# Kernel tuning notes

Measured on AMD Instinct MI355X. Metric: run time of the kernel, lower is better.

## Reference

```python
import jax, jax.numpy as jnp
import numpy as np

M = 2_097_152
C = 32
R = 256

# Same plane_axes buffer as the torch module (3 permutation matrices).
PLANE_AXES = jnp.array(
    [[[0, 1, 0], [1, 0, 0], [0, 0, 1]],
     [[0, 0, 1], [1, 0, 0], [0, 1, 0]],
     [[0, 1, 0], [0, 0, 1], [1, 0, 0]]], dtype=jnp.float32)


def setup_inputs() -> dict:
    key = jax.random.key(0)
    k1, k2 = jax.random.split(key)
    xyz = jax.random.uniform(k1, (M, 3), dtype=jnp.float32, minval=-1.0, maxval=1.0)
    # rand_init: triplane = randn * 0.001
    triplane = jax.random.normal(k2, (3, C, R, R), dtype=jnp.float32) * 0.001
    return {"xyz": xyz, "triplane": triplane}


def _grid_sample_bilinear(plane, coords):
    """plane: (C,H,W); coords: (M,2) normalized (x,y) in [-1,1].
    Matches torch F.grid_sample(mode='bilinear', padding_mode='zeros',
    align_corners=True). Returns (M,C)."""
    Cc, H, W = plane.shape
    ix = (coords[:, 0] + 1.0) * 0.5 * (W - 1)  # x indexes width
    iy = (coords[:, 1] + 1.0) * 0.5 * (H - 1)  # y indexes height
    x0 = jnp.floor(ix)
    y0 = jnp.floor(iy)
    x1 = x0 + 1.0
    y1 = y0 + 1.0
    wx1 = ix - x0
    wx0 = 1.0 - wx1
    wy1 = iy - y0
    wy0 = 1.0 - wy1

    def tap(xf, yf, w):
        valid = (xf >= 0) & (xf <= W - 1) & (yf >= 0) & (yf <= H - 1)
        xi = jnp.clip(xf, 0, W - 1).astype(jnp.int32)
        yi = jnp.clip(yf, 0, H - 1).astype(jnp.int32)
        v = plane[:, yi, xi]  # (C, M) gather
        return v * (w * valid.astype(w.dtype))[None, :]

    out = (tap(x0, y0, wx0 * wy0) + tap(x1, y0, wx1 * wy0)
           + tap(x0, y1, wx0 * wy1) + tap(x1, y1, wx1 * wy1))  # (C, M)
    return out.T  # (M, C)


def reference(xyz, triplane):
    # project_onto_planes: xyz @ inv(plane_axes), keep first two coords
    inv_planes = jnp.linalg.inv(PLANE_AXES)             # (3,3,3)
    proj = jnp.einsum('md,pdk->pmk', xyz, inv_planes)[..., :2]  # (3,M,2)
    feats = jax.vmap(_grid_sample_bilinear)(triplane, proj)      # (3,M,C)
    return feats.sum(axis=0)  # (M,C)
```

## Files before the change

### kernel.cpp

```cpp
#include <hip/hip_runtime.h>

#define R 256
#define C 32
#define NBIN 512
#define CAPB 6144
#define PPB 1024
#define CNTP 16
#define SUBC 64

typedef float f32x4 __attribute__((ext_vector_type(4)));

__device__ __forceinline__ void bin_key_of(float px, float py, float pz,
                                           int& bin, int& key) {
    int gx = min(max((int)((px + 1.0f) * 16.0f), 0), 31);
    int gy = min(max((int)((py + 1.0f) * 16.0f), 0), 31);
    int gz = min(max((int)((pz + 1.0f) * 16.0f), 0), 31);
    int bx = gx >> 2, by = gy >> 2, bz = gz >> 2;
    int oct = ((bz >> 2) << 2) | ((by >> 2) << 1) | (bx >> 2);
    int sub = ((bz & 3) << 4) | ((by & 3) << 2) | (bx & 3);
    bin = (sub << 3) | oct;
    key = ((gz & 3) << 4) | ((gy & 3) << 2) | (gx & 3);
}

__device__ __forceinline__ void convert_body(const float* __restrict__ tri,
                                             ushort* __restrict__ tw, int bid) {
    int p = bid >> 8;
    int y = bid & (R - 1);
    int x = threadIdx.x;

    unsigned packed[C / 2];
#pragma unroll
    for (int i = 0; i < C / 2; ++i) {
        unsigned w = 0;
#pragma unroll
        for (int h = 0; h < 2; ++h) {
            float f = tri[(((p * C + (2 * i + h)) * R) + y) * R + x];
            unsigned u = __float_as_uint(f);
            unsigned r = (u + 0x7fffu + ((u >> 16) & 1u)) >> 16;
            w |= (r & 0xffffu) << (16 * h);
        }
        packed[i] = w;
    }
    uint4* dst = (uint4*)(tw + ((size_t)(p * R + y) * R + x) * C);
#pragma unroll
    for (int i = 0; i < 4; ++i) {
        dst[i] = make_uint4(packed[4 * i], packed[4 * i + 1],
                            packed[4 * i + 2], packed[4 * i + 3]);
    }
}

__global__ __launch_bounds__(256) void convert_scatter_kernel(
        const float* __restrict__ tri, ushort* __restrict__ tw,
        const float* __restrict__ xyz, unsigned* __restrict__ acnt,
        unsigned* __restrict__ ovcnt, f32x4* __restrict__ arena,
        f32x4* __restrict__ ov, int M) {
    int bid = blockIdx.x;
    if (bid < 3 * R) {
        convert_body(tri, tw, bid);
        return;
    }

    __shared__ unsigned lcnt[NBIN], lbase[NBIN], gbase[NBIN], lofs[NBIN];
    __shared__ f32x4 stag[PPB];
    __shared__ ushort sbin[PPB];

    int t = threadIdx.x;
    for (int c = t; c < NBIN; c += 256) { lcnt[c] = 0u; lofs[c] = 0u; }
    __syncthreads();

    int base = (bid - 3 * R) * PPB;
    float pxl[4], pyl[4], pzl[4];
    int   bl[4], kl[4];
#pragma unroll
    for (int k = 0; k < 4; ++k) {
        int m = base + k * 256 + t;
        bl[k] = -1;
        if (m < M) {
            pxl[k] = xyz[3 * m + 0];
            pyl[k] = xyz[3 * m + 1];
            pzl[k] = xyz[3 * m + 2];
            bin_key_of(pxl[k], pyl[k], pzl[k], bl[k], kl[k]);
            atomicAdd(&lcnt[bl[k]], 1u);
        }
    }
    __syncthreads();

    if (t < 64) {
        unsigned run = 0;
        for (int c = 0; c < NBIN; c += 64) {
            unsigned x   = lcnt[c + t];
            unsigned inc = x;
#pragma unroll
            for (int d = 1; d < 64; d <<= 1) {
                unsigned v = __shfl_up(inc, d);
                if (t >= d) inc += v;
            }
            lbase[c + t] = run + inc - x;
            run += __shfl(inc, 63);
        }
    }
    __syncthreads();

    for (int c = t; c < NBIN; c += 256) {
        unsigned x = lcnt[c];
        if (x) gbase[c] = atomicAdd(&acnt[c * CNTP], x);
    }
    __syncthreads();

#pragma unroll
    for (int k = 0; k < 4; ++k) {
        if (bl[k] >= 0) {
            unsigned j = lbase[bl[k]] + atomicAdd(&lofs[bl[k]], 1u);
            int m = base + k * 256 + t;
            f32x4 rec = {pxl[k], pyl[k], pzl[k],
                         __int_as_float((kl[k] << 21) | m)};
            stag[j] = rec;
            sbin[j] = (ushort)bl[k];
        }
    }
    __syncthreads();

    int tot = (int)(lbase[NBIN - 1] + lcnt[NBIN - 1]);
    for (int j = t; j < tot; j += 256) {
        int b = sbin[j];
        unsigned pos = gbase[b] + ((unsigned)j - lbase[b]);
        f32x4 rec = stag[j];
        if (pos < CAPB) arena[(size_t)b * CAPB + pos] = rec;
        else            ov[atomicAdd(ovcnt, 1u)] = rec;
    }
}

__global__ __launch_bounds__(256) void convert_kernel(const float* __restrict__ tri,
                                                      ushort* __restrict__ tw) {
    convert_body(tri, tw, blockIdx.x);
}

__device__ __forceinline__ void tap_fma(uint4 v, float w, float* acc) {
    unsigned d[4] = {v.x, v.y, v.z, v.w};
#pragma unroll
    for (int k = 0; k < 4; ++k) {
        acc[2 * k]     = fmaf(w, __uint_as_float(d[k] << 16),          acc[2 * k]);
        acc[2 * k + 1] = fmaf(w, __uint_as_float(d[k] & 0xffff0000u), acc[2 * k + 1]);
    }
}

__device__ __forceinline__ void sample_point(float px, float py, float pz, int mo,
                                             const ushort* __restrict__ twc,
                                             float* __restrict__ out, int cq) {
    float uu[3] = {py, pz, py};
    float vv[3] = {px, px, pz};

    uint4 v[12];
    float wt[12];
#pragma unroll
    for (int p = 0; p < 3; ++p) {
        float ix = (uu[p] + 1.0f) * 0.5f * 255.0f;
        float iy = (vv[p] + 1.0f) * 0.5f * 255.0f;
        int   x0 = (int)ix;
        int   y0 = (int)iy;
        float wx1 = ix - (float)x0;
        float wy1 = iy - (float)y0;
        float wx0 = 1.0f - wx1;
        float wy0 = 1.0f - wy1;
        int x1 = min(x0 + 1, R - 1);
        int y1 = min(y0 + 1, R - 1);

        const ushort* pl = twc + (size_t)p * R * R * C;
        v[4 * p + 0] = *(const uint4*)(pl + (y0 * R + x0) * C);
        v[4 * p + 1] = *(const uint4*)(pl + (y0 * R + x1) * C);
        v[4 * p + 2] = *(const uint4*)(pl + (y1 * R + x0) * C);
        v[4 * p + 3] = *(const uint4*)(pl + (y1 * R + x1) * C);
        wt[4 * p + 0] = wx0 * wy0;
        wt[4 * p + 1] = wx1 * wy0;
        wt[4 * p + 2] = wx0 * wy1;
        wt[4 * p + 3] = wx1 * wy1;
    }

    float acc[8];
#pragma unroll
    for (int j = 0; j < 8; ++j) acc[j] = 0.0f;
#pragma unroll
    for (int s = 0; s < 12; ++s) tap_fma(v[s], wt[s], acc);

    f32x4* o = (f32x4*)(out + (size_t)mo * C + 8 * cq);
    f32x4 o0 = {acc[0], acc[1], acc[2], acc[3]};
    f32x4 o1 = {acc[4], acc[5], acc[6], acc[7]};
    __builtin_nontemporal_store(o0, o);
    __builtin_nontemporal_store(o1, o + 1);
}

__global__ __launch_bounds__(512, 4) void sample_bins(
        const f32x4* __restrict__ arena, const unsigned* __restrict__ acnt,
        const unsigned* __restrict__ ovcnt, const f32x4* __restrict__ ov,
        const ushort* __restrict__ tw, float* __restrict__ out) {
    __shared__ unsigned char skey[CAPB];
    __shared__ ushort        sidx[CAPB];
    __shared__ unsigned      scnt[SUBC], sbase[SUBC], sofs[SUBC];

    int bin = blockIdx.x;
    int t   = threadIdx.x;

    if (t < SUBC) { scnt[t] = 0u; sofs[t] = 0u; }
    __syncthreads();

    int n = min((int)acnt[bin * CNTP], CAPB);
    const f32x4* bk = arena + (size_t)bin * CAPB;

    for (int i = t; i < n; i += 512) {
        int bits = __float_as_int(bk[i].w);
        int k    = (bits >> 21) & 63;
        skey[i]  = (unsigned char)k;
        atomicAdd(&scnt[k], 1u);
    }
    __syncthreads();

    if (t < 64) {
        unsigned x   = scnt[t];
        unsigned inc = x;
#pragma unroll
        for (int d = 1; d < 64; d <<= 1) {
            unsigned v = __shfl_up(inc, d);
            if (t >= d) inc += v;
        }
        sbase[t] = inc - x;
    }
    __syncthreads();

    for (int i = t; i < n; i += 512) {
        int k = skey[i];
        unsigned pos = sbase[k] + atomicAdd(&sofs[k], 1u);
        sidx[pos] = (ushort)i;
    }
    __syncthreads();

    int quad = t >> 2;
    int cq   = t & 3;
    const ushort* twc = tw + 8 * cq;

    for (int j0 = 0; j0 < n; j0 += 128) {
        int j = j0 + quad;
        if (j < n) {
            f32x4 r = bk[sidx[j]];
            int mo = __float_as_int(r.w) & 0x1FFFFF;
            sample_point(r.x, r.y, r.z, mo, twc, out, cq);
        }
    }

    int nov = (int)*ovcnt;
    if (nov > 0) {
        int gq = (bin * 512 + t) >> 2;
        for (int j = gq; j < nov; j += 512 * 128) {
            f32x4 r = ov[j];
            int mo = __float_as_int(r.w) & 0x1FFFFF;
            sample_point(r.x, r.y, r.z, mo, twc, out, cq);
        }
    }
}

__global__ __launch_bounds__(256) void sample_kernel(const float* __restrict__ xyz,
                                                     const ushort* __restrict__ tw,
                                                     float* __restrict__ out, int M) {
    int tid = blockIdx.x * 256 + threadIdx.x;
    int q   = tid >> 2;
    int cq  = tid & 3;
    int nq  = (gridDim.x * 256) >> 2;
    const ushort* twc = tw + 8 * cq;
    for (int m = q; m < M; m += nq) {
        float px = xyz[3 * m + 0], py = xyz[3 * m + 1], pz = xyz[3 * m + 2];
        sample_point(px, py, pz, m, twc, out, cq);
    }
}

extern "C" void kernel_launch(void* const* d_in, const int* in_sizes, int n_in,
                              void* d_out, int out_size, void* d_ws, size_t ws_size,
                              hipStream_t stream) {
    const float* xyz = (const float*)d_in[0];
    const float* tri = (const float*)d_in[1];
    float* out = (float*)d_out;

    int M = in_sizes[0] / 3;

    size_t tw_bytes  = (size_t)3 * R * R * C * sizeof(ushort);
    size_t cnt_off   = tw_bytes;
    size_t cnt_bytes = (size_t)NBIN * CNTP * sizeof(unsigned) + 128;
    size_t arena_off = cnt_off + ((cnt_bytes + 255) & ~(size_t)255);
    size_t ov_off    = arena_off + (size_t)NBIN * CAPB * sizeof(f32x4);
    size_t need      = ov_off + (size_t)M * sizeof(f32x4);

    ushort*   tw    = (ushort*)d_ws;
    unsigned* acnt  = (unsigned*)((char*)d_ws + cnt_off);
    unsigned* ovcnt = acnt + NBIN * CNTP;
    f32x4*    arena = (f32x4*)((char*)d_ws + arena_off);
    f32x4*    ov    = (f32x4*)((char*)d_ws + ov_off);

    if (ws_size >= need) {
        hipMemsetAsync(acnt, 0, cnt_bytes, stream);
        int sb = (M + PPB - 1) / PPB;
        convert_scatter_kernel<<<3 * R + sb, 256, 0, stream>>>(
            tri, tw, xyz, acnt, ovcnt, arena, ov, M);
        sample_bins<<<NBIN, 512, 0, stream>>>(arena, acnt, ovcnt, ov, tw, out);
    } else {
        convert_kernel<<<3 * R, 256, 0, stream>>>(tri, tw);
        sample_kernel<<<4096, 256, 0, stream>>>(xyz, tw, out, M);
    }
}
```

Measured before the change: 437.1 us.

## Stage sorted bin records in LDS and enlarge scatter blocks to 1024 threads

The binning pass now uses 1024-thread blocks that each handle 4096 points, and triplane conversion covers four rows per block. This cuts the number of global bin-counter atomics and produces longer contiguous runs when writing to the arena. The sampling kernel now copies full records into shared memory in sub-key order, rather than keeping an index array and re-reading the arena from global memory at random. In exchange, both kernels use much more LDS (about 74 KB for the sampler's record buffer), which can lower occupancy. Bins larger than the shared capacity fall back to unsorted processing, and the fast path now also requires M to be a multiple of 4096.

```diff
diff --git a/kernel.cpp b/kernel.cpp
--- a/kernel.cpp
+++ b/kernel.cpp
@@ -4,9 +4,10 @@
 #define C 32
 #define NBIN 512
 #define CAPB 6144
-#define PPB 1024
+#define PPB 4096
 #define CNTP 16
 #define SUBC 64
+#define SCAP 4608
 
 typedef float f32x4 __attribute__((ext_vector_type(4)));
 
@@ -22,12 +23,11 @@
     key = ((gz & 3) << 4) | ((gy & 3) << 2) | (gx & 3);
 }
 
-__device__ __forceinline__ void convert_body(const float* __restrict__ tri,
-                                             ushort* __restrict__ tw, int bid) {
-    int p = bid >> 8;
-    int y = bid & (R - 1);
-    int x = threadIdx.x;
-
+__device__ __forceinline__ void convert_row(const float* __restrict__ tri,
+                                            ushort* __restrict__ tw,
+                                            int row, int x) {
+    int p = row >> 8;
+    int y = row & (R - 1);
     unsigned packed[C / 2];
 #pragma unroll
     for (int i = 0; i < C / 2; ++i) {
@@ -41,7 +41,7 @@
         }
         packed[i] = w;
     }
-    uint4* dst = (uint4*)(tw + ((size_t)(p * R + y) * R + x) * C);
+    uint4* dst = (uint4*)(tw + ((size_t)row * R + x) * C);
 #pragma unroll
     for (int i = 0; i < 4; ++i) {
         dst[i] = make_uint4(packed[4 * i], packed[4 * i + 1],
@@ -49,14 +49,16 @@
     }
 }
 
-__global__ __launch_bounds__(256) void convert_scatter_kernel(
+__global__ __launch_bounds__(1024) void convert_scatter_kernel(
         const float* __restrict__ tri, ushort* __restrict__ tw,
         const float* __restrict__ xyz, unsigned* __restrict__ acnt,
         unsigned* __restrict__ ovcnt, f32x4* __restrict__ arena,
         f32x4* __restrict__ ov, int M) {
     int bid = blockIdx.x;
-    if (bid < 3 * R) {
-        convert_body(tri, tw, bid);
+    int t   = threadIdx.x;
+
+    if (bid < 3 * R / 4) {
+        convert_row(tri, tw, bid * 4 + (t >> 8), t & (R - 1));
         return;
     }
 
@@ -64,16 +66,15 @@
     __shared__ f32x4 stag[PPB];
     __shared__ ushort sbin[PPB];
 
-    int t = threadIdx.x;
-    for (int c = t; c < NBIN; c += 256) { lcnt[c] = 0u; lofs[c] = 0u; }
-    __syncthreads();
-
-    int base = (bid - 3 * R) * PPB;
+    for (int c = t; c < NBIN; c += 1024) { lcnt[c] = 0u; lofs[c] = 0u; }
+    __syncthreads();
+
+    int base = (bid - 3 * R / 4) * PPB;
     float pxl[4], pyl[4], pzl[4];
     int   bl[4], kl[4];
 #pragma unroll
     for (int k = 0; k < 4; ++k) {
-        int m = base + k * 256 + t;
+        int m = base + k * 1024 + t;
         bl[k] = -1;
         if (m < M) {
             pxl[k] = xyz[3 * m + 0];
@@ -101,9 +102,9 @@
     }
     __syncthreads();
 
-    for (int c = t; c < NBIN; c += 256) {
-        unsigned x = lcnt[c];
-        if (x) gbase[c] = atomicAdd(&acnt[c * CNTP], x);
+    if (t < NBIN) {
+        unsigned x = lcnt[t];
+        if (x) gbase[t] = atomicAdd(&acnt[t * CNTP], x);
     }
     __syncthreads();
 
@@ -111,7 +112,7 @@
     for (int k = 0; k < 4; ++k) {
         if (bl[k] >= 0) {
             unsigned j = lbase[bl[k]] + atomicAdd(&lofs[bl[k]], 1u);
-            int m = base + k * 256 + t;
+            int m = base + k * 1024 + t;
             f32x4 rec = {pxl[k], pyl[k], pzl[k],
                          __int_as_float((kl[k] << 21) | m)};
             stag[j] = rec;
@@ -121,7 +122,7 @@
     __syncthreads();
 
     int tot = (int)(lbase[NBIN - 1] + lcnt[NBIN - 1]);
-    for (int j = t; j < tot; j += 256) {
+    for (int j = t; j < tot; j += 1024) {
         int b = sbin[j];
         unsigned pos = gbase[b] + ((unsigned)j - lbase[b]);
         f32x4 rec = stag[j];
@@ -132,7 +133,7 @@
 
 __global__ __launch_bounds__(256) void convert_kernel(const float* __restrict__ tri,
                                                       ushort* __restrict__ tw) {
-    convert_body(tri, tw, blockIdx.x);
+    convert_row(tri, tw, blockIdx.x, threadIdx.x);
 }
 
 __device__ __forceinline__ void tap_fma(uint4 v, float w, float* acc) {
@@ -193,9 +194,8 @@
         const f32x4* __restrict__ arena, const unsigned* __restrict__ acnt,
         const unsigned* __restrict__ ovcnt, const f32x4* __restrict__ ov,
         const ushort* __restrict__ tw, float* __restrict__ out) {
-    __shared__ unsigned char skey[CAPB];
-    __shared__ ushort        sidx[CAPB];
-    __shared__ unsigned      scnt[SUBC], sbase[SUBC], sofs[SUBC];
+    __shared__ f32x4    srec[SCAP];
+    __shared__ unsigned scnt[SUBC], sbase[SUBC], sofs[SUBC];
 
     int bin = blockIdx.x;
     int t   = threadIdx.x;
@@ -205,44 +205,54 @@
 
     int n = min((int)acnt[bin * CNTP], CAPB);
     const f32x4* bk = arena + (size_t)bin * CAPB;
-
-    for (int i = t; i < n; i += 512) {
-        int bits = __float_as_int(bk[i].w);
-        int k    = (bits >> 21) & 63;
-        skey[i]  = (unsigned char)k;
-        atomicAdd(&scnt[k], 1u);
-    }
-    __syncthreads();
-
-    if (t < 64) {
-        unsigned x   = scnt[t];
-        unsigned inc = x;
-#pragma unroll
-        for (int d = 1; d < 64; d <<= 1) {
-            unsigned v = __shfl_up(inc, d);
-            if (t >= d) inc += v;
-        }
-        sbase[t] = inc - x;
-    }
-    __syncthreads();
-
-    for (int i = t; i < n; i += 512) {
-        int k = skey[i];
-        unsigned pos = sbase[k] + atomicAdd(&sofs[k], 1u);
-        sidx[pos] = (ushort)i;
-    }
-    __syncthreads();
 
     int quad = t >> 2;
     int cq   = t & 3;
     const ushort* twc = tw + 8 * cq;
 
-    for (int j0 = 0; j0 < n; j0 += 128) {
-        int j = j0 + quad;
-        if (j < n) {
-            f32x4 r = bk[sidx[j]];
-            int mo = __float_as_int(r.w) & 0x1FFFFF;
-            sample_point(r.x, r.y, r.z, mo, twc, out, cq);
+    if (n <= SCAP) {
+        for (int i = t; i < n; i += 512) {
+            int k = (__float_as_int(bk[i].w) >> 21) & 63;
+            atomicAdd(&scnt[k], 1u);
+        }
+        __syncthreads();
+
+        if (t < 64) {
+            unsigned x   = scnt[t];
+            unsigned inc = x;
+#pragma unroll
+            for (int d = 1; d < 64; d <<= 1) {
+                unsigned v = __shfl_up(inc, d);
+                if (t >= d) inc += v;
+            }
+            sbase[t] = inc - x;
+        }
+        __syncthreads();
+
+        for (int i = t; i < n; i += 512) {
+            f32x4 rec = bk[i];
+            int k = (__float_as_int(rec.w) >> 21) & 63;
+            unsigned pos = sbase[k] + atomicAdd(&sofs[k], 1u);
+            srec[pos] = rec;
+        }
+        __syncthreads();
+
+        for (int j0 = 0; j0 < n; j0 += 128) {
+            int j = j0 + quad;
+            if (j < n) {
+                f32x4 r = srec[j];
+                int mo = __float_as_int(r.w) & 0x1FFFFF;
+                sample_point(r.x, r.y, r.z, mo, twc, out, cq);
+            }
+        }
+    } else {
+        for (int j0 = 0; j0 < n; j0 += 128) {
+            int j = j0 + quad;
+            if (j < n) {
+                f32x4 r = bk[j];
+                int mo = __float_as_int(r.w) & 0x1FFFFF;
+                sample_point(r.x, r.y, r.z, mo, twc, out, cq);
+            }
         }
     }
 
@@ -293,10 +303,10 @@
     f32x4*    arena = (f32x4*)((char*)d_ws + arena_off);
     f32x4*    ov    = (f32x4*)((char*)d_ws + ov_off);
 
-    if (ws_size >= need) {
+    if (ws_size >= need && (M % PPB) == 0) {
         hipMemsetAsync(acnt, 0, cnt_bytes, stream);
-        int sb = (M + PPB - 1) / PPB;
-        convert_scatter_kernel<<<3 * R + sb, 256, 0, stream>>>(
+        int sb = M / PPB;
+        convert_scatter_kernel<<<3 * R / 4 + sb, 1024, 0, stream>>>(
             tri, tw, xyz, acnt, ovcnt, arena, ov, M);
         sample_bins<<<NBIN, 512, 0, stream>>>(arena, acnt, ovcnt, ov, tw, out);
     } else {
```

New measurement: 376.4 us. -13.9%, faster.
